# Optimization experiments

Hardware: AMD Instinct MI355X
Metric: run time of the kernel (lower is better)

Reference implementation:

```python
import jax, jax.numpy as jnp
import numpy as np

N_NODES = 50000


def setup_inputs() -> dict:
    key = jax.random.key(0)
    ks = jax.random.split(key, 10)
    B, N, D, H, O = 2, N_NODES, 128, 128, 10
    x = jax.random.normal(ks[0], (B, N, D), dtype=jnp.float32)
    edge_index = jax.random.randint(ks[1], (2, 800000), 0, N, dtype=jnp.int32)
    s = lambda fan_in: 1.0 / np.sqrt(fan_in)
    W  = jax.random.uniform(ks[2], (D, H), jnp.float32, -s(D), s(D))
    b  = jnp.zeros((H,), jnp.float32)
    W1 = jax.random.uniform(ks[3], (H, H // 2), jnp.float32, -s(H), s(H))
    b1 = jnp.zeros((H // 2,), jnp.float32)
    W2 = jax.random.uniform(ks[4], (H // 2, H // 4), jnp.float32, -s(H // 2), s(H // 2))
    b2 = jnp.zeros((H // 4,), jnp.float32)
    W3 = jax.random.uniform(ks[5], (H // 4, O), jnp.float32, -s(H // 4), s(H // 4))
    b3 = jnp.zeros((O,), jnp.float32)
    return {"x": x, "edge_index": edge_index, "W": W, "b": b,
            "W1": W1, "b1": b1, "W2": W2, "b2": b2, "W3": W3, "b3": b3}


def reference(x, edge_index, W, b, W1, b1, W2, b2, W3, b3):
    # GraphConvolution (Kipf): support = x @ W; out[dst] += support[src]; + b
    src, dst = edge_index[0], edge_index[1]
    support = jnp.einsum("bnd,dh->bnh", x, W)          # [B, N, H]
    msgs = support[:, src, :]                            # [B, E, H] gather
    agg = jnp.zeros_like(support).at[:, dst, :].add(msgs)  # scatter-add
    h = jax.nn.gelu(agg + b, approximate=False)          # GELU (torch default erf)
    # dropout is identity at inference (training=False)
    h = jax.nn.relu(jnp.einsum("bnh,hk->bnk", h, W1) + b1)
    h = jax.nn.relu(jnp.einsum("bnk,km->bnm", h, W2) + b2)
    h = jnp.einsum("bnm,mo->bno", h, W3) + b3            # [B, N, O]
    return h.mean(axis=1)                                # [B, O]
```

## Files before the change

kernel.cpp:

```cpp
#include <hip/hip_runtime.h>
#include <math.h>

#define NN 50000
#define DD 128
#define HH 128
#define L1 64
#define L2 32
#define OO 10

#define NW0 16384
#define NW1 8192
#define NW2 2048

typedef short v8s __attribute__((ext_vector_type(8)));
typedef float v4f __attribute__((ext_vector_type(4)));

__device__ __forceinline__ float bf2f_lo(unsigned u) { return __uint_as_float(u << 16); }
__device__ __forceinline__ float bf2f_hi(unsigned u) { return __uint_as_float(u & 0xffff0000u); }
__device__ __forceinline__ unsigned short f2bf(float f) {
    unsigned u = __float_as_uint(f);
    return (unsigned short)((u + 0x7fffu + ((u >> 16) & 1u)) >> 16);
}
__device__ __forceinline__ unsigned pack2(float lo, float hi) {
    return (unsigned)f2bf(lo) | ((unsigned)f2bf(hi) << 16);
}
__device__ __forceinline__ float gelu_f(float v) {
    return 0.5f * v * (1.f + erff(v * 0.70710678118654752f));
}

__global__ __launch_bounds__(256) void k_wprep(
    const float* __restrict__ W, const float* __restrict__ W1,
    const float* __restrict__ W2, unsigned short* __restrict__ wtp,
    unsigned short* __restrict__ w1tp, unsigned short* __restrict__ w2tp)
{
    int i = blockIdx.x * 256 + threadIdx.x;
    if (i < NW0) {
        const int e = i & 7, ln = (i >> 3) & 63, ks = (i >> 9) & 3, ct = i >> 11;
        wtp[i] = f2bf(W[(ks * 32 + (ln >> 4) * 8 + e) * HH + ct * 16 + (ln & 15)]);
    } else if (i < NW0 + NW1) {
        const int j = i - NW0;
        const int e = j & 7, ln = (j >> 3) & 63, ks = (j >> 9) & 3, ct = j >> 11;
        w1tp[j] = f2bf(W1[(ks * 32 + (ln >> 4) * 8 + e) * L1 + ct * 16 + (ln & 15)]);
    } else if (i < NW0 + NW1 + NW2) {
        const int j = i - NW0 - NW1;
        const int e = j & 7, ln = (j >> 3) & 63, ks = (j >> 9) & 1, ct = j >> 10;
        w2tp[j] = f2bf(W2[(ks * 32 + (ln >> 4) * 8 + e) * L2 + ct * 16 + (ln & 15)]);
    }
}

__global__ __launch_bounds__(256) void k_xcvt(
    const float* __restrict__ x, unsigned short* __restrict__ xb,
    const int* __restrict__ ei, int* __restrict__ counts, int E)
{
    const int gid = blockIdx.x * 256 + threadIdx.x;
    const int stride = gridDim.x * 256;
    const int HALF = NN * 32;
    for (int idx = gid; idx < 2 * HALF; idx += stride) {
        const int b = (idx >= HALF) ? 1 : 0;
        const int j = idx - b * HALF;
        const int n = j >> 5;
        const int c4 = j & 31;
        const float4 v = *(const float4*)(x + ((size_t)b * NN + n) * DD + c4 * 4);
        ushort4 o;
        o.x = f2bf(v.x); o.y = f2bf(v.y); o.z = f2bf(v.z); o.w = f2bf(v.w);
        *(ushort4*)(xb + ((size_t)n * 2 + b) * DD + c4 * 4) = o;
    }
    for (int e = gid; e < E; e += stride)
        atomicAdd(&counts[ei[(size_t)E + e]], 1);
}

__global__ __launch_bounds__(1024) void k_scan1(
    const int* __restrict__ counts, int* __restrict__ offsets,
    int* __restrict__ blksum, int n)
{
    __shared__ int wsum[16], woff[16];
    const int tid = threadIdx.x, lane = tid & 63, wv = tid >> 6;
    const int i = blockIdx.x * 1024 + tid;
    int v = (i < n) ? counts[i] : 0;
    int x = v;
    #pragma unroll
    for (int d = 1; d < 64; d <<= 1) { int t = __shfl_up(x, d); if (lane >= d) x += t; }
    if (lane == 63) wsum[wv] = x;
    __syncthreads();
    if (wv == 0 && lane < 16) {
        int y = wsum[lane];
        #pragma unroll
        for (int d = 1; d < 16; d <<= 1) { int t = __shfl_up(y, d); if (lane >= d) y += t; }
        woff[lane] = y - wsum[lane];
        if (lane == 15) blksum[blockIdx.x] = y;
    }
    __syncthreads();
    if (i < n) offsets[i] = woff[wv] + (x - v);
}

__global__ __launch_bounds__(1024) void k_scan2(
    int* __restrict__ offsets, const int* __restrict__ blksum, int nblk, int n)
{
    __shared__ int base_sh, tot_sh;
    const int tid = threadIdx.x, lane = tid & 63, wv = tid >> 6;
    if (wv == 0) {
        int v = (lane < nblk) ? blksum[lane] : 0;
        int x = v;
        #pragma unroll
        for (int d = 1; d < 64; d <<= 1) { int t = __shfl_up(x, d); if (lane >= d) x += t; }
        int incl = __shfl(x, blockIdx.x);
        int own  = __shfl(v, blockIdx.x);
        int tot  = __shfl(x, nblk - 1);
        if (lane == 0) { base_sh = incl - own; tot_sh = tot; }
    }
    __syncthreads();
    const int i = blockIdx.x * 1024 + tid;
    if (i < n) offsets[i] += base_sh;
    if (blockIdx.x == nblk - 1 && tid == 0) offsets[n] = tot_sh;
}

__global__ __launch_bounds__(256) void k_bucket(
    const int* __restrict__ ei, const int* __restrict__ offsets,
    int* __restrict__ cursor, int* __restrict__ ss, int E)
{
    int e = blockIdx.x * 256 + threadIdx.x;
    if (e < E) {
        int d = ei[E + e];
        int pos = offsets[d] + atomicAdd(&cursor[d], 1);
        ss[pos] = ei[e];
    }
}

template<bool FUSED>
__global__ __launch_bounds__(512, 6) void k_mlp_t(
    const unsigned short* __restrict__ src,
    const int* __restrict__ offsets, const int* __restrict__ ss,
    const unsigned short* __restrict__ wtp, const float* __restrict__ b0v,
    const unsigned short* __restrict__ w1tp, const float* __restrict__ b1v,
    const unsigned short* __restrict__ w2tp, const float* __restrict__ b2v,
    float* __restrict__ partials, int srows)
{
    __shared__ __align__(16) unsigned char upool[64 * 136 * 2];
    __shared__ __align__(16) unsigned short h1b[64 * 72];
    __shared__ float b0s[DD], b1s[L1], b2s[L2];
    __shared__ float oacc[64];
    unsigned short* xa  = (unsigned short*)upool;
    unsigned short* hsb = (unsigned short*)upool;
    float* h2p = (float*)upool;

    const int tid = threadIdx.x;
    const int row0 = blockIdx.x * 64;
    const int lane = tid & 63;
    const int w = tid >> 6;

    if (tid < DD) b0s[tid] = b0v[tid];
    if (tid < L1) b1s[tid] = b1v[tid];
    if (tid < L2) b2s[tid] = b2v[tid];
    if (tid < 64) oacc[tid] = 0.f;

    if (FUSED) {
        const int sel = (lane < 32) ? 0 : 1;
        const int co = (lane & 31) * 8;
        #pragma unroll
        for (int j = 0; j < 4; ++j) {
            const int ln = w * 4 + j;
            const int d = blockIdx.x * 32 + ln;
            const int s0 = (d < NN) ? offsets[d] : 0;
            const int s1 = (d < NN) ? offsets[d + 1] : 0;
            float a[8];
            #pragma unroll
            for (int t = 0; t < 8; ++t) a[t] = 0.f;
            int i = s0;
            for (; i + 4 <= s1; i += 4) {
                const int sA = ss[i + sel];
                const int sB = ss[i + 2 + sel];
                const uint4 ra = *(const uint4*)(src + (size_t)sA * 256 + co);
                const uint4 rb = *(const uint4*)(src + (size_t)sB * 256 + co);
                a[0] += bf2f_lo(ra.x); a[1] += bf2f_hi(ra.x);
                a[2] += bf2f_lo(ra.y); a[3] += bf2f_hi(ra.y);
                a[4] += bf2f_lo(ra.z); a[5] += bf2f_hi(ra.z);
                a[6] += bf2f_lo(ra.w); a[7] += bf2f_hi(ra.w);
                a[0] += bf2f_lo(rb.x); a[1] += bf2f_hi(rb.x);
                a[2] += bf2f_lo(rb.y); a[3] += bf2f_hi(rb.y);
                a[4] += bf2f_lo(rb.z); a[5] += bf2f_hi(rb.z);
                a[6] += bf2f_lo(rb.w); a[7] += bf2f_hi(rb.w);
            }
            if (i + 2 <= s1) {
                const int sA = ss[i + sel];
                const uint4 ra = *(const uint4*)(src + (size_t)sA * 256 + co);
                a[0] += bf2f_lo(ra.x); a[1] += bf2f_hi(ra.x);
                a[2] += bf2f_lo(ra.y); a[3] += bf2f_hi(ra.y);
                a[4] += bf2f_lo(ra.z); a[5] += bf2f_hi(ra.z);
                a[6] += bf2f_lo(ra.w); a[7] += bf2f_hi(ra.w);
                i += 2;
            }
            if (i < s1 && lane < 32) {
                const int sA = ss[i];
                const uint4 ra = *(const uint4*)(src + (size_t)sA * 256 + co);
                a[0] += bf2f_lo(ra.x); a[1] += bf2f_hi(ra.x);
                a[2] += bf2f_lo(ra.y); a[3] += bf2f_hi(ra.y);
                a[4] += bf2f_lo(ra.z); a[5] += bf2f_hi(ra.z);
                a[6] += bf2f_lo(ra.w); a[7] += bf2f_hi(ra.w);
            }
            #pragma unroll
            for (int t = 0; t < 8; ++t) a[t] += __shfl_xor(a[t], 32);
            if (lane < 32) {
                const int tr = ln * 2 + (lane >> 4);
                const int col = (lane & 15) * 8;
                uint4 o;
                o.x = pack2(a[0], a[1]); o.y = pack2(a[2], a[3]);
                o.z = pack2(a[4], a[5]); o.w = pack2(a[6], a[7]);
                *(uint4*)(&xa[tr * 136 + col]) = o;
            }
        }
    } else {
        for (int u = tid * 8; u < 64 * DD; u += 4096) {
            const int r = u >> 7, c = u & 127;
            uint4 raw = make_uint4(0, 0, 0, 0);
            if (row0 + r < srows) raw = *(const uint4*)(src + (size_t)(row0 + r) * HH + c);
            *(uint4*)(&xa[r * 136 + c]) = raw;
        }
    }
    __syncthreads();

    const int lm = lane & 15;
    const int q = lane >> 4;
    const int r1 = (w & 3) * 16;
    const int ch = w >> 2;

    {
        v4f acc[4];
        #pragma unroll
        for (int i = 0; i < 4; ++i) acc[i] = (v4f)(0.f);
        #pragma unroll
        for (int ks = 0; ks < 4; ++ks) {
            const int k0 = ks * 32 + q * 8;
            const v8s af = *(const v8s*)(&xa[(r1 + lm) * 136 + k0]);
            #pragma unroll
            for (int ct = 0; ct < 4; ++ct) {
                const int ctg = ch * 4 + ct;
                const v8s bf = *(const v8s*)(wtp + ((size_t)(ctg * 4 + ks) * 64 + lane) * 8);
                acc[ct] = __builtin_amdgcn_mfma_f32_16x16x32_bf16(af, bf, acc[ct], 0, 0, 0);
            }
        }
        __syncthreads();

        #pragma unroll
        for (int ct = 0; ct < 4; ++ct) {
            const int col = ch * 64 + ct * 16 + lm;
            const float bias = b0s[col];
            #pragma unroll
            for (int r = 0; r < 4; ++r)
                hsb[(r1 + q * 4 + r) * 136 + col] = f2bf(gelu_f(acc[ct][r] + bias));
        }
    }
    __syncthreads();

    {
        v4f a1[2];
        a1[0] = (v4f)(0.f); a1[1] = (v4f)(0.f);
        #pragma unroll
        for (int ks = 0; ks < 4; ++ks) {
            const int k0 = ks * 32 + q * 8;
            const v8s af = *(const v8s*)(&hsb[(r1 + lm) * 136 + k0]);
            #pragma unroll
            for (int ct = 0; ct < 2; ++ct) {
                const int ctg = ch * 2 + ct;
                const v8s bf = *(const v8s*)(w1tp + ((size_t)(ctg * 4 + ks) * 64 + lane) * 8);
                a1[ct] = __builtin_amdgcn_mfma_f32_16x16x32_bf16(af, bf, a1[ct], 0, 0, 0);
            }
        }
        #pragma unroll
        for (int ct = 0; ct < 2; ++ct) {
            const int col = ch * 32 + ct * 16 + lm;
            const float bias = b1s[col];
            #pragma unroll
            for (int r = 0; r < 4; ++r)
                h1b[(r1 + q * 4 + r) * 72 + col] = f2bf(fmaxf(a1[ct][r] + bias, 0.f));
        }
    }
    __syncthreads();

    {
        v4f a2 = (v4f)(0.f);
        #pragma unroll
        for (int ks = 0; ks < 2; ++ks) {
            const int k0 = ks * 32 + q * 8;
            const v8s af = *(const v8s*)(&h1b[(r1 + lm) * 72 + k0]);
            const v8s bf = *(const v8s*)(w2tp + ((size_t)(ch * 2 + ks) * 64 + lane) * 8);
            a2 = __builtin_amdgcn_mfma_f32_16x16x32_bf16(af, bf, a2, 0, 0, 0);
        }
        __syncthreads();
        const int col = ch * 16 + lm;
        const float bias = b2s[col];
        #pragma unroll
        for (int r = 0; r < 4; ++r)
            h2p[(r1 + q * 4 + r) * 36 + col] = fmaxf(a2[r] + bias, 0.f);
    }
    __syncthreads();

    {
        const int c = tid & 31;
        const int g = tid >> 5;
        float p0 = 0.f, p1 = 0.f;
        #pragma unroll
        for (int i = 0; i < 4; ++i) {
            const int r = g * 4 + i;
            if (row0 + r < srows) {
                const float v = h2p[r * 36 + c];
                if (r & 1) p1 += v; else p0 += v;
            }
        }
        if (p0 != 0.f) atomicAdd(&oacc[c], p0);
        if (p1 != 0.f) atomicAdd(&oacc[32 + c], p1);
    }
    __syncthreads();
    if (tid < 64) partials[(size_t)blockIdx.x * 64 + tid] = oacc[tid];
}

__global__ __launch_bounds__(256) void k_scatter(
    const int* __restrict__ ei, const unsigned short* __restrict__ xb,
    float* __restrict__ aggf, int E)
{
    const int tid = threadIdx.x;
    const int eg = tid >> 6;
    const int lane = tid & 63;
    const int e = blockIdx.x * 4 + eg;
    if (e >= E) return;
    const int src = ei[e];
    const int dst = ei[E + e];
    const uint2 r = *(const uint2*)(xb + (size_t)src * 256 + lane * 4);
    float* ap = aggf + (size_t)dst * 256 + lane * 4;
    unsafeAtomicAdd(ap + 0, bf2f_lo(r.x));
    unsafeAtomicAdd(ap + 1, bf2f_hi(r.x));
    unsafeAtomicAdd(ap + 2, bf2f_lo(r.y));
    unsafeAtomicAdd(ap + 3, bf2f_hi(r.y));
}

__global__ __launch_bounds__(256) void k_cvt(
    const float* __restrict__ in, unsigned short* __restrict__ outb, int n)
{
    int i = blockIdx.x * 256 + threadIdx.x;
    if (i < n) outb[i] = f2bf(in[i]);
}

__global__ __launch_bounds__(256) void k_reduce(
    const float* __restrict__ partials, float* __restrict__ accum, int nblk)
{
    __shared__ float lsum[4][64];
    const int t = threadIdx.x & 63;
    const int w = threadIdx.x >> 6;
    float s = 0.f;
    for (int g = blockIdx.x * 4 + w; g < nblk; g += gridDim.x * 4)
        s += partials[(size_t)g * 64 + t];
    lsum[w][t] = s;
    __syncthreads();
    if (threadIdx.x < 64) {
        const float v = lsum[0][t] + lsum[1][t] + lsum[2][t] + lsum[3][t];
        unsafeAtomicAdd(&accum[t], v);
    }
}

__global__ __launch_bounds__(64) void k_final(
    const float* __restrict__ accum, const float* __restrict__ W3,
    const float* __restrict__ b3v, float* __restrict__ out)
{
    const int tid = threadIdx.x;
    if (tid < 2 * OO) {
        const int b = tid / OO, o = tid % OO;
        float acc = b3v[o];
        const float inv = 1.0f / (float)NN;
        #pragma unroll
        for (int j = 0; j < L2; ++j) acc += (accum[b * 32 + j] * inv) * W3[j * OO + o];
        out[tid] = acc;
    }
}

extern "C" void kernel_launch(void* const* d_in, const int* in_sizes, int n_in,
                              void* d_out, int out_size, void* d_ws, size_t ws_size,
                              hipStream_t stream) {
    const float* x  = (const float*)d_in[0];
    const int*   ei = (const int*)d_in[1];
    const float* W  = (const float*)d_in[2];
    const float* b0 = (const float*)d_in[3];
    const float* W1 = (const float*)d_in[4];
    const float* b1 = (const float*)d_in[5];
    const float* W2 = (const float*)d_in[6];
    const float* b2 = (const float*)d_in[7];
    const float* W3 = (const float*)d_in[8];
    const float* b3 = (const float*)d_in[9];
    float* out = (float*)d_out;

    const int E = in_sizes[1] / 2;
    const int rows = 2 * NN;
    const int nblk = (rows + 63) / 64;
    const int nsb = (NN + 1023) / 1024;
    const int wpn = NW0 + NW1 + NW2;

    unsigned short* xb   = (unsigned short*)d_ws;
    unsigned short* aggb = xb + (size_t)rows * HH;
    float* partials = (float*)(aggb + (size_t)rows * HH);
    float* accum    = partials + (size_t)nblk * 64;
    int*   counts   = (int*)(accum + 64);
    int*   cursor   = counts + NN;
    int*   offsets  = cursor + NN;
    int*   blksum   = offsets + NN + 1;
    unsigned short* wtp = (unsigned short*)(((uintptr_t)(blksum + 64) + 15) & ~(uintptr_t)15);
    unsigned short* w1tp = wtp + NW0;
    unsigned short* w2tp = w1tp + NW1;
    int*   ss       = (int*)(w2tp + NW2);
    float* aggf     = (float*)(ss + E);
    const size_t need_csr = ((size_t)rows * HH * 2 + wpn) * sizeof(unsigned short)
                      + ((size_t)nblk * 64 + 64) * sizeof(float)
                      + ((size_t)NN * 3 + 1 + 64 + E) * sizeof(int) + 16;
    const size_t need_fb = need_csr + (size_t)rows * HH * sizeof(float);

    if (ws_size >= need_csr && nsb <= 64) {
        hipMemsetAsync(accum, 0, (64 + 2 * (size_t)NN) * sizeof(int), stream);
        k_wprep<<<dim3((wpn + 255) / 256), dim3(256), 0, stream>>>(W, W1, W2, wtp, w1tp, w2tp);
        k_xcvt<<<dim3(2048), dim3(256), 0, stream>>>(x, xb, ei, counts, E);
        k_scan1<<<dim3(nsb), dim3(1024), 0, stream>>>(counts, offsets, blksum, NN);
        k_scan2<<<dim3(nsb), dim3(1024), 0, stream>>>(offsets, blksum, nsb, NN);
        k_bucket<<<dim3((E + 255) / 256), dim3(256), 0, stream>>>(ei, offsets, cursor, ss, E);
        k_mlp_t<true><<<dim3(nblk), dim3(512), 0, stream>>>(
            xb, offsets, ss, wtp, b0, w1tp, b1, w2tp, b2, partials, rows);
    } else if (ws_size >= need_fb) {
        hipMemsetAsync(accum, 0, 64 * sizeof(float), stream);
        hipMemsetAsync(aggf, 0, (size_t)rows * HH * sizeof(float), stream);
        k_wprep<<<dim3((wpn + 255) / 256), dim3(256), 0, stream>>>(W, W1, W2, wtp, w1tp, w2tp);
        k_xcvt<<<dim3(2048), dim3(256), 0, stream>>>(x, xb, ei, counts, 0);
        k_scatter<<<dim3((E + 3) / 4), dim3(256), 0, stream>>>(ei, xb, aggf, E);
        k_cvt<<<dim3((rows * HH + 255) / 256), dim3(256), 0, stream>>>(aggf, aggb, rows * HH);
        k_mlp_t<false><<<dim3(nblk), dim3(512), 0, stream>>>(
            aggb, offsets, ss, wtp, b0, w1tp, b1, w2tp, b2, partials, rows);
    }

    k_reduce<<<dim3(64), dim3(256), 0, stream>>>(partials, accum, nblk);
    k_final<<<dim3(1), dim3(64), 0, stream>>>(accum, W3, b3, out);
}
```

Measured before the change: 263.8 us.

## Pad CSR buckets to multiples of eight and fuse prep and reduce kernels

Each node's edge count is rounded up to a multiple of eight, and the padding slots are filled with a sentinel index that points at a zero row. This lets the aggregation loop load four source indices as a single vector and issue four gathers per half-wave with no tail handling. The weight-prep and x-conversion kernels are merged into one launch, and the reduce and final kernels are merged using a last-block atomic counter, which removes launches. In exchange, padding adds extra gather traffic, up to seven wasted rows per node, and the workspace layout changes.

```diff
diff --git a/kernel.cpp b/kernel.cpp
--- a/kernel.cpp
+++ b/kernel.cpp
@@ -11,6 +11,7 @@
 #define NW0 16384
 #define NW1 8192
 #define NW2 2048
+#define NWT (NW0 + NW1 + NW2)
 
 typedef short v8s __attribute__((ext_vector_type(8)));
 typedef float v4f __attribute__((ext_vector_type(4)));
@@ -28,32 +29,33 @@
     return 0.5f * v * (1.f + erff(v * 0.70710678118654752f));
 }
 
-__global__ __launch_bounds__(256) void k_wprep(
+__global__ __launch_bounds__(256) void k_prep(
+    const float* __restrict__ x, unsigned short* __restrict__ xb,
+    const int* __restrict__ ei, int* __restrict__ counts,
     const float* __restrict__ W, const float* __restrict__ W1,
     const float* __restrict__ W2, unsigned short* __restrict__ wtp,
-    unsigned short* __restrict__ w1tp, unsigned short* __restrict__ w2tp)
-{
-    int i = blockIdx.x * 256 + threadIdx.x;
-    if (i < NW0) {
-        const int e = i & 7, ln = (i >> 3) & 63, ks = (i >> 9) & 3, ct = i >> 11;
-        wtp[i] = f2bf(W[(ks * 32 + (ln >> 4) * 8 + e) * HH + ct * 16 + (ln & 15)]);
-    } else if (i < NW0 + NW1) {
-        const int j = i - NW0;
-        const int e = j & 7, ln = (j >> 3) & 63, ks = (j >> 9) & 3, ct = j >> 11;
-        w1tp[j] = f2bf(W1[(ks * 32 + (ln >> 4) * 8 + e) * L1 + ct * 16 + (ln & 15)]);
-    } else if (i < NW0 + NW1 + NW2) {
-        const int j = i - NW0 - NW1;
-        const int e = j & 7, ln = (j >> 3) & 63, ks = (j >> 9) & 1, ct = j >> 10;
-        w2tp[j] = f2bf(W2[(ks * 32 + (ln >> 4) * 8 + e) * L2 + ct * 16 + (ln & 15)]);
-    }
-}
-
-__global__ __launch_bounds__(256) void k_xcvt(
-    const float* __restrict__ x, unsigned short* __restrict__ xb,
-    const int* __restrict__ ei, int* __restrict__ counts, int E)
+    unsigned short* __restrict__ w1tp, unsigned short* __restrict__ w2tp,
+    int* __restrict__ ssf, int nfill, unsigned* __restrict__ zrow, int E)
 {
     const int gid = blockIdx.x * 256 + threadIdx.x;
     const int stride = gridDim.x * 256;
+
+    for (int i = gid; i < NWT; i += stride) {
+        if (i < NW0) {
+            const int e = i & 7, ln = (i >> 3) & 63, ks = (i >> 9) & 3, ct = i >> 11;
+            wtp[i] = f2bf(W[(ks * 32 + (ln >> 4) * 8 + e) * HH + ct * 16 + (ln & 15)]);
+        } else if (i < NW0 + NW1) {
+            const int j = i - NW0;
+            const int e = j & 7, ln = (j >> 3) & 63, ks = (j >> 9) & 3, ct = j >> 11;
+            w1tp[j] = f2bf(W1[(ks * 32 + (ln >> 4) * 8 + e) * L1 + ct * 16 + (ln & 15)]);
+        } else {
+            const int j = i - NW0 - NW1;
+            const int e = j & 7, ln = (j >> 3) & 63, ks = (j >> 9) & 1, ct = j >> 10;
+            w2tp[j] = f2bf(W2[(ks * 32 + (ln >> 4) * 8 + e) * L2 + ct * 16 + (ln & 15)]);
+        }
+    }
+    if (zrow != nullptr && gid < 128) zrow[gid] = 0u;
+    for (int i = gid; i < nfill; i += stride) ssf[i] = NN;
     const int HALF = NN * 32;
     for (int idx = gid; idx < 2 * HALF; idx += stride) {
         const int b = (idx >= HALF) ? 1 : 0;
@@ -76,7 +78,7 @@
     __shared__ int wsum[16], woff[16];
     const int tid = threadIdx.x, lane = tid & 63, wv = tid >> 6;
     const int i = blockIdx.x * 1024 + tid;
-    int v = (i < n) ? counts[i] : 0;
+    int v = (i < n) ? ((counts[i] + 7) & ~7) : 0;
     int x = v;
     #pragma unroll
     for (int d = 1; d < 64; d <<= 1) { int t = __shfl_up(x, d); if (lane >= d) x += t; }
@@ -154,48 +156,39 @@
     if (tid < 64) oacc[tid] = 0.f;
 
     if (FUSED) {
-        const int sel = (lane < 32) ? 0 : 1;
+        const int half4 = (lane >> 5) * 4;
         const int co = (lane & 31) * 8;
         #pragma unroll
         for (int j = 0; j < 4; ++j) {
             const int ln = w * 4 + j;
             const int d = blockIdx.x * 32 + ln;
-            const int s0 = (d < NN) ? offsets[d] : 0;
-            const int s1 = (d < NN) ? offsets[d + 1] : 0;
+            int s0 = 0, s1 = 0;
+            if (d < NN) { s0 = offsets[d]; s1 = offsets[d + 1]; }
             float a[8];
             #pragma unroll
             for (int t = 0; t < 8; ++t) a[t] = 0.f;
-            int i = s0;
-            for (; i + 4 <= s1; i += 4) {
-                const int sA = ss[i + sel];
-                const int sB = ss[i + 2 + sel];
-                const uint4 ra = *(const uint4*)(src + (size_t)sA * 256 + co);
-                const uint4 rb = *(const uint4*)(src + (size_t)sB * 256 + co);
-                a[0] += bf2f_lo(ra.x); a[1] += bf2f_hi(ra.x);
-                a[2] += bf2f_lo(ra.y); a[3] += bf2f_hi(ra.y);
-                a[4] += bf2f_lo(ra.z); a[5] += bf2f_hi(ra.z);
-                a[6] += bf2f_lo(ra.w); a[7] += bf2f_hi(ra.w);
-                a[0] += bf2f_lo(rb.x); a[1] += bf2f_hi(rb.x);
-                a[2] += bf2f_lo(rb.y); a[3] += bf2f_hi(rb.y);
-                a[4] += bf2f_lo(rb.z); a[5] += bf2f_hi(rb.z);
-                a[6] += bf2f_lo(rb.w); a[7] += bf2f_hi(rb.w);
-            }
-            if (i + 2 <= s1) {
-                const int sA = ss[i + sel];
-                const uint4 ra = *(const uint4*)(src + (size_t)sA * 256 + co);
-                a[0] += bf2f_lo(ra.x); a[1] += bf2f_hi(ra.x);
-                a[2] += bf2f_lo(ra.y); a[3] += bf2f_hi(ra.y);
-                a[4] += bf2f_lo(ra.z); a[5] += bf2f_hi(ra.z);
-                a[6] += bf2f_lo(ra.w); a[7] += bf2f_hi(ra.w);
-                i += 2;
-            }
-            if (i < s1 && lane < 32) {
-                const int sA = ss[i];
-                const uint4 ra = *(const uint4*)(src + (size_t)sA * 256 + co);
-                a[0] += bf2f_lo(ra.x); a[1] += bf2f_hi(ra.x);
-                a[2] += bf2f_lo(ra.y); a[3] += bf2f_hi(ra.y);
-                a[4] += bf2f_lo(ra.z); a[5] += bf2f_hi(ra.z);
-                a[6] += bf2f_lo(ra.w); a[7] += bf2f_hi(ra.w);
+            for (int i = s0; i < s1; i += 8) {
+                const uint4 idx = *(const uint4*)(ss + i + half4);
+                const uint4 r0 = *(const uint4*)(src + (size_t)idx.x * 256 + co);
+                const uint4 r1 = *(const uint4*)(src + (size_t)idx.y * 256 + co);
+                const uint4 r2 = *(const uint4*)(src + (size_t)idx.z * 256 + co);
+                const uint4 r3 = *(const uint4*)(src + (size_t)idx.w * 256 + co);
+                a[0] += bf2f_lo(r0.x); a[1] += bf2f_hi(r0.x);
+                a[2] += bf2f_lo(r0.y); a[3] += bf2f_hi(r0.y);
+                a[4] += bf2f_lo(r0.z); a[5] += bf2f_hi(r0.z);
+                a[6] += bf2f_lo(r0.w); a[7] += bf2f_hi(r0.w);
+                a[0] += bf2f_lo(r1.x); a[1] += bf2f_hi(r1.x);
+                a[2] += bf2f_lo(r1.y); a[3] += bf2f_hi(r1.y);
+                a[4] += bf2f_lo(r1.z); a[5] += bf2f_hi(r1.z);
+                a[6] += bf2f_lo(r1.w); a[7] += bf2f_hi(r1.w);
+                a[0] += bf2f_lo(r2.x); a[1] += bf2f_hi(r2.x);
+                a[2] += bf2f_lo(r2.y); a[3] += bf2f_hi(r2.y);
+                a[4] += bf2f_lo(r2.z); a[5] += bf2f_hi(r2.z);
+                a[6] += bf2f_lo(r2.w); a[7] += bf2f_hi(r2.w);
+                a[0] += bf2f_lo(r3.x); a[1] += bf2f_hi(r3.x);
+                a[2] += bf2f_lo(r3.y); a[3] += bf2f_hi(r3.y);
+                a[4] += bf2f_lo(r3.z); a[5] += bf2f_hi(r3.z);
+                a[6] += bf2f_lo(r3.w); a[7] += bf2f_hi(r3.w);
             }
             #pragma unroll
             for (int t = 0; t < 8; ++t) a[t] += __shfl_xor(a[t], 32);
@@ -339,10 +332,13 @@
     if (i < n) outb[i] = f2bf(in[i]);
 }
 
-__global__ __launch_bounds__(256) void k_reduce(
-    const float* __restrict__ partials, float* __restrict__ accum, int nblk)
+__global__ __launch_bounds__(256) void k_reduce_final(
+    const float* __restrict__ partials, float* __restrict__ accum, int nblk,
+    int* __restrict__ dcnt, const float* __restrict__ W3,
+    const float* __restrict__ b3v, float* __restrict__ out)
 {
     __shared__ float lsum[4][64];
+    __shared__ int lastf;
     const int t = threadIdx.x & 63;
     const int w = threadIdx.x >> 6;
     float s = 0.f;
@@ -354,20 +350,19 @@
         const float v = lsum[0][t] + lsum[1][t] + lsum[2][t] + lsum[3][t];
         unsafeAtomicAdd(&accum[t], v);
     }
-}
-
-__global__ __launch_bounds__(64) void k_final(
-    const float* __restrict__ accum, const float* __restrict__ W3,
-    const float* __restrict__ b3v, float* __restrict__ out)
-{
-    const int tid = threadIdx.x;
-    if (tid < 2 * OO) {
-        const int b = tid / OO, o = tid % OO;
+    __threadfence();
+    __syncthreads();
+    if (threadIdx.x == 0)
+        lastf = (atomicAdd(dcnt, 1) == (int)gridDim.x - 1) ? 1 : 0;
+    __syncthreads();
+    if (lastf && threadIdx.x < 2 * OO) {
+        const int b = threadIdx.x / OO, o = threadIdx.x % OO;
         float acc = b3v[o];
         const float inv = 1.0f / (float)NN;
         #pragma unroll
-        for (int j = 0; j < L2; ++j) acc += (accum[b * 32 + j] * inv) * W3[j * OO + o];
-        out[tid] = acc;
+        for (int j = 0; j < L2; ++j)
+            acc += (unsafeAtomicAdd(&accum[b * 32 + j], 0.f) * inv) * W3[j * OO + o];
+        out[threadIdx.x] = acc;
     }
 }
 
@@ -390,46 +385,56 @@
     const int rows = 2 * NN;
     const int nblk = (rows + 63) / 64;
     const int nsb = (NN + 1023) / 1024;
-    const int wpn = NW0 + NW1 + NW2;
-
-    unsigned short* xb   = (unsigned short*)d_ws;
-    unsigned short* aggb = xb + (size_t)rows * HH;
-    float* partials = (float*)(aggb + (size_t)rows * HH);
+    const int SSN = E + 7 * NN + 8;
+
+    unsigned short* xb = (unsigned short*)d_ws;
+    unsigned* zrow     = (unsigned*)(xb + (size_t)rows * HH);
+    int*   ss       = (int*)(zrow + 128);
+    float* partials = (float*)(ss + SSN);
     float* accum    = partials + (size_t)nblk * 64;
-    int*   counts   = (int*)(accum + 64);
+    int*   dcnt     = (int*)(accum + 64);
+    int*   counts   = dcnt + 16;
     int*   cursor   = counts + NN;
     int*   offsets  = cursor + NN;
     int*   blksum   = offsets + NN + 1;
     unsigned short* wtp = (unsigned short*)(((uintptr_t)(blksum + 64) + 15) & ~(uintptr_t)15);
     unsigned short* w1tp = wtp + NW0;
     unsigned short* w2tp = w1tp + NW1;
-    int*   ss       = (int*)(w2tp + NW2);
-    float* aggf     = (float*)(ss + E);
-    const size_t need_csr = ((size_t)rows * HH * 2 + wpn) * sizeof(unsigned short)
-                      + ((size_t)nblk * 64 + 64) * sizeof(float)
-                      + ((size_t)NN * 3 + 1 + 64 + E) * sizeof(int) + 16;
-    const size_t need_fb = need_csr + (size_t)rows * HH * sizeof(float);
+    const size_t need_csr = (size_t)((unsigned short*)(w2tp + NW2) - (unsigned short*)d_ws)
+                            * sizeof(unsigned short) + 16;
+
+    unsigned short* f_aggb = xb + (size_t)rows * HH;
+    float* f_partials = (float*)(f_aggb + (size_t)rows * HH);
+    float* f_accum    = f_partials + (size_t)nblk * 64;
+    int*   f_dcnt     = (int*)(f_accum + 64);
+    unsigned short* f_wtp = (unsigned short*)(((uintptr_t)(f_dcnt + 16) + 15) & ~(uintptr_t)15);
+    unsigned short* f_w1tp = f_wtp + NW0;
+    unsigned short* f_w2tp = f_w1tp + NW1;
+    float* f_aggf     = (float*)(((uintptr_t)(f_w2tp + NW2) + 15) & ~(uintptr_t)15);
+    const size_t need_fb = (size_t)((char*)(f_aggf + (size_t)rows * HH) - (char*)d_ws) + 16;
 
     if (ws_size >= need_csr && nsb <= 64) {
-        hipMemsetAsync(accum, 0, (64 + 2 * (size_t)NN) * sizeof(int), stream);
-        k_wprep<<<dim3((wpn + 255) / 256), dim3(256), 0, stream>>>(W, W1, W2, wtp, w1tp, w2tp);
-        k_xcvt<<<dim3(2048), dim3(256), 0, stream>>>(x, xb, ei, counts, E);
+        hipMemsetAsync(accum, 0, (80 + 2 * (size_t)NN) * sizeof(int), stream);
+        k_prep<<<dim3(2048), dim3(256), 0, stream>>>(
+            x, xb, ei, counts, W, W1, W2, wtp, w1tp, w2tp, ss, SSN, zrow, E);
         k_scan1<<<dim3(nsb), dim3(1024), 0, stream>>>(counts, offsets, blksum, NN);
         k_scan2<<<dim3(nsb), dim3(1024), 0, stream>>>(offsets, blksum, nsb, NN);
         k_bucket<<<dim3((E + 255) / 256), dim3(256), 0, stream>>>(ei, offsets, cursor, ss, E);
         k_mlp_t<true><<<dim3(nblk), dim3(512), 0, stream>>>(
             xb, offsets, ss, wtp, b0, w1tp, b1, w2tp, b2, partials, rows);
+        k_reduce_final<<<dim3(64), dim3(256), 0, stream>>>(
+            partials, accum, nblk, dcnt, W3, b3, out);
     } else if (ws_size >= need_fb) {
-        hipMemsetAsync(accum, 0, 64 * sizeof(float), stream);
-        hipMemsetAsync(aggf, 0, (size_t)rows * HH * sizeof(float), stream);
-        k_wprep<<<dim3((wpn + 255) / 256), dim3(256), 0, stream>>>(W, W1, W2, wtp, w1tp, w2tp);
-        k_xcvt<<<dim3(2048), dim3(256), 0, stream>>>(x, xb, ei, counts, 0);
-        k_scatter<<<dim3((E + 3) / 4), dim3(256), 0, stream>>>(ei, xb, aggf, E);
-        k_cvt<<<dim3((rows * HH + 255) / 256), dim3(256), 0, stream>>>(aggf, aggb, rows * HH);
+        hipMemsetAsync(f_accum, 0, 80 * sizeof(int), stream);
+        hipMemsetAsync(f_aggf, 0, (size_t)rows * HH * sizeof(float), stream);
+        k_prep<<<dim3(2048), dim3(256), 0, stream>>>(
+            x, xb, ei, (int*)f_dcnt , W, W1, W2, f_wtp, f_w1tp, f_w2tp,
+            (int*)f_dcnt, 0, nullptr, 0);
+        k_scatter<<<dim3((E + 3) / 4), dim3(256), 0, stream>>>(ei, xb, f_aggf, E);
+        k_cvt<<<dim3((rows * HH + 255) / 256), dim3(256), 0, stream>>>(f_aggf, f_aggb, rows * HH);
         k_mlp_t<false><<<dim3(nblk), dim3(512), 0, stream>>>(
-            aggb, offsets, ss, wtp, b0, w1tp, b1, w2tp, b2, partials, rows);
-    }
-
-    k_reduce<<<dim3(64), dim3(256), 0, stream>>>(partials, accum, nblk);
-    k_final<<<dim3(1), dim3(64), 0, stream>>>(accum, W3, b3, out);
-}
+            f_aggb, nullptr, nullptr, f_wtp, b0, f_w1tp, b1, f_w2tp, b2, f_partials, rows);
+        k_reduce_final<<<dim3(64), dim3(256), 0, stream>>>(
+            f_partials, f_accum, nblk, f_dcnt, W3, b3, out);
+    }
+}
```

Measured after the change: 273.4 us. +3.6%, slower.
